# Performance work log

Measured on AMD Instinct MI355X. Metric: run time of the kernel, lower is better.

The kernel has to match this reference:

```python
import jax, jax.numpy as jnp
import numpy as np

N = 65536      # total nodes
B = 128        # graphs in batch
NP = 512       # nodes per graph (N = B*NP)
E = 524288     # edges, avg degree 8, kept within-graph
DIN = 128      # input feature dim
C = 256        # hidden channels
H = 4          # attention heads
DH = C // H
EPS_NRM = 1e-12  # F.normalize eps (SAGEConv normalize=True)
EPS = 1e-5       # GraphNorm / LayerNorm eps


def _xavier(k, shape):
    lim = np.sqrt(6.0 / (shape[-1] + shape[-2]))
    return jax.random.uniform(k, shape, jnp.float32, -lim, lim)


def setup_inputs() -> dict:
    key = jax.random.key(0)
    ks = jax.random.split(key, 20)
    g = jnp.arange(E) // (E // B)  # graph id per edge
    src = (jax.random.randint(ks[0], (E,), 0, NP) + g * NP).astype(jnp.int32)
    dst = (jax.random.randint(ks[1], (E,), 0, NP) + g * NP).astype(jnp.int32)
    edge_index = jnp.stack([src, dst])
    batch = (jnp.arange(N) // NP).astype(jnp.int32)
    x = jax.random.normal(ks[2], (N, DIN), jnp.float32)
    return dict(
        x=x, edge_index=edge_index, batch=batch,
        l0_lin_l_w=_xavier(ks[3], (C, DIN)), l0_lin_l_b=jnp.zeros((C,), jnp.float32),
        l0_lin_r_w=_xavier(ks[4], (C, DIN)),
        l0_res_w=_xavier(ks[5], (C, DIN)),
        lin_l_w=jnp.stack([_xavier(ks[6 + i], (C, C)) for i in range(3)]),
        lin_l_b=jnp.zeros((3, C), jnp.float32),
        lin_r_w=jnp.stack([_xavier(ks[9 + i], (C, C)) for i in range(3)]),
        gn_w=jnp.ones((4, C), jnp.float32), gn_b=jnp.zeros((4, C), jnp.float32),
        gn_alpha=jnp.ones((4, C), jnp.float32),
        attn_in_w=_xavier(ks[12], (3 * C, C)), attn_in_b=jnp.zeros((3 * C,), jnp.float32),
        attn_out_w=_xavier(ks[13], (C, C)), attn_out_b=jnp.zeros((C,), jnp.float32),
        ln_w=jnp.ones((C,), jnp.float32), ln_b=jnp.zeros((C,), jnp.float32),
        pool_w=_xavier(ks[14], (C, 3 * C)), pool_b=jnp.zeros((C,), jnp.float32),
    )


def _forward(x, src, dst, batch, p):
    (l0_lin_l_w, l0_lin_l_b, l0_lin_r_w, l0_res_w, lin_l_w, lin_l_b, lin_r_w,
     gn_w, gn_b, gn_alpha, attn_in_w, attn_in_b, attn_out_w, attn_out_b,
     ln_w, ln_b, pool_w, pool_b) = p
    gelu = lambda v: jax.nn.gelu(v, approximate=False)  # torch nn.GELU default (erf)
    deg = jnp.maximum(jax.ops.segment_sum(jnp.ones((E,), x.dtype), dst, num_segments=N), 1.0)[:, None]

    def sage(h, w_l, b_l, w_r):
        # SAGEConv(mean aggr, normalize=True): lin_l(mean_j x_j) + lin_r(x_i), then L2-normalize
        agg = jax.ops.segment_sum(h[src], dst, num_segments=N) / deg
        out = agg @ w_l.T + b_l + h @ w_r.T
        return out / jnp.maximum(jnp.linalg.norm(out, axis=-1, keepdims=True), EPS_NRM)

    def graph_norm(h, w, b, alpha):
        # GraphNorm: w * (h - alpha*mean_g) / sqrt(var_g + eps) + b, per-graph per-channel
        mean = (jax.ops.segment_sum(h, batch, num_segments=B) / NP)[batch]
        out = h - alpha * mean
        var = (jax.ops.segment_sum(out * out, batch, num_segments=B) / NP)[batch]
        return w * out / jnp.sqrt(var + EPS) + b

    # GNN blocks (eval mode: dropout = identity); layer 0 has residual projection DIN->C
    h = gelu(graph_norm(sage(x, l0_lin_l_w, l0_lin_l_b, l0_lin_r_w), gn_w[0], gn_b[0], gn_alpha[0]))
    x1 = h + x @ l0_res_w.T
    for i in range(3):
        h = gelu(graph_norm(sage(x1, lin_l_w[i], lin_l_b[i], lin_r_w[i]), gn_w[i + 1], gn_b[i + 1], gn_alpha[i + 1]))
        x1 = h + x1

    # BatchedAttentionBlock: equal-size graphs -> to_dense_batch is a reshape, mask all-true
    xd = x1.reshape(B, NP, C)
    qkv = xd @ attn_in_w.T + attn_in_b
    q, k, v = jnp.split(qkv, 3, axis=-1)
    to_h = lambda t: t.reshape(B, NP, H, DH).transpose(0, 2, 1, 3)
    q, k, v = to_h(q), to_h(k), to_h(v)
    scores = jnp.einsum('bhqd,bhkd->bhqk', q, k) / np.float32(np.sqrt(DH))
    attn = jax.nn.softmax(scores, axis=-1)
    o = jnp.einsum('bhqk,bhkd->bhqd', attn, v).transpose(0, 2, 1, 3).reshape(B, NP, C)
    o = o @ attn_out_w.T + attn_out_b
    x2 = o.reshape(N, C) + x1

    # LayerNorm(mode='graph'): normalize over all nodes*features of each graph
    xg = x2.reshape(B, NP * C)
    mu = xg.mean(axis=1, keepdims=True)
    cen = xg - mu
    var = (cen * cen).mean(axis=1, keepdims=True)
    x3 = gelu((cen / jnp.sqrt(var + EPS)).reshape(N, C) * ln_w + ln_b)

    # multi-pool (mean/max/sum) + projection -> graph embedding [B, C]
    xp = x3.reshape(B, NP, C)
    pooled = jnp.concatenate([xp.mean(1), xp.max(1), xp.sum(1)], axis=1)
    return pooled @ pool_w.T + pool_b


def reference(x, edge_index, batch, l0_lin_l_w, l0_lin_l_b, l0_lin_r_w, l0_res_w,
              lin_l_w, lin_l_b, lin_r_w, gn_w, gn_b, gn_alpha,
              attn_in_w, attn_in_b, attn_out_w, attn_out_b, ln_w, ln_b, pool_w, pool_b):
    src, dst = edge_index[0], edge_index[1]
    p = (l0_lin_l_w, l0_lin_l_b, l0_lin_r_w, l0_res_w, lin_l_w, lin_l_b, lin_r_w,
         gn_w, gn_b, gn_alpha, attn_in_w, attn_in_b, attn_out_w, attn_out_b,
         ln_w, ln_b, pool_w, pool_b)
    return _forward(x, src, dst, batch, p)
```

## Files before the change

kernel.cpp:

```cpp
#include <hip/hip_runtime.h>


#define N_TOT   65536
#define B_GR    128
#define NP_     512
#define E_TOT   524288
#define EPG     4096
#define DIN_    128
#define C_      256
#define C3_     768
#define H_      4

typedef unsigned int uint;
typedef unsigned short ushort;

#define O_L0LW  0u
#define O_L0LB  32768u
#define O_L0RW  33024u
#define O_L0RES 65792u
#define O_LWL   98560u
#define O_LBL   295168u
#define O_LWR   295936u
#define O_GNW   492544u
#define O_GNB   493568u
#define O_GNA   494592u
#define O_AIW   495616u
#define O_AIB   692224u
#define O_AOW   692992u
#define O_AOB   758528u
#define O_LNW   758784u
#define O_LNB   759040u
#define O_PLW   759296u
#define O_PLB   955904u
#define TOTALP  956160u

typedef __attribute__((ext_vector_type(8))) short bf16x8_t;
typedef __attribute__((ext_vector_type(4))) float f32x4_t;

__device__ __forceinline__ float bf2f(ushort u){ union{uint i; float f;} v; v.i = ((uint)u) << 16; return v.f; }
__device__ __forceinline__ ushort f2bf(float f){
  union{float f; uint u;} v; v.f = f;
  uint u = v.u;
  u += 0x7fffu + ((u >> 16) & 1u);
  return (ushort)(u >> 16);
}
__device__ __forceinline__ uint pack2(float a, float b){ return (uint)f2bf(a) | ((uint)f2bf(b) << 16); }
__device__ __forceinline__ float u2f_lo(uint u){ union{uint i; float f;} v; v.i = u << 16; return v.f; }
__device__ __forceinline__ float u2f_hi(uint u){ union{uint i; float f;} v; v.i = u & 0xffff0000u; return v.f; }
__device__ __forceinline__ float gelu_f(float x){ return 0.5f * x * (1.0f + erff(x * 0.70710678118654752440f)); }
__device__ __forceinline__ float wredsum(float v){
  #pragma unroll
  for (int off = 32; off; off >>= 1) v += __shfl_xor(v, off, 64);
  return v;
}

__global__ void probe_dtype(const uint* __restrict__ gnw_raw, uint* __restrict__ flag){
  if (threadIdx.x == 0 && blockIdx.x == 0)
    *flag = (gnw_raw[0] == 0x3F800000u) ? 1u : 0u;
}

struct Seg { const void* p; uint ofs; };
struct CvtArgs { Seg s[19]; };

__global__ __launch_bounds__(256) void cvt_params(CvtArgs a, ushort* __restrict__ pb,
                                                  const uint* __restrict__ flag){
  uint gi = blockIdx.x * 256u + threadIdx.x;
  if (gi >= TOTALP) return;
  int lo = 0;
  #pragma unroll
  for (int s = 1; s < 18; ++s) if (gi >= a.s[s].ofs) lo = s;
  uint rel = gi - a.s[lo].ofs;
  pb[gi] = (*flag) ? f2bf(((const float*)a.s[lo].p)[rel]) : ((const ushort*)a.s[lo].p)[rel];
}

__global__ __launch_bounds__(256) void cvt_flat(const void* __restrict__ in, ushort* __restrict__ out,
                                                const uint* __restrict__ flag){
  uint i = blockIdx.x * 256u + threadIdx.x;
  out[i] = (*flag) ? f2bf(((const float*)in)[i]) : ((const ushort*)in)[i];
}

__global__ void deg_count(const int* __restrict__ dst, uint* __restrict__ deg){
  int e = blockIdx.x * 256 + threadIdx.x;
  atomicAdd(&deg[dst[e]], 1u);
}

__global__ __launch_bounds__(512) void scan_deg(const uint* __restrict__ deg,
    uint* __restrict__ rowptr, uint* __restrict__ cursor)
{
  __shared__ uint s[512];
  const int g = blockIdx.x, tid = threadIdx.x;
  uint v = deg[g * NP_ + tid];
  s[tid] = v;
  __syncthreads();
  #pragma unroll
  for (int off = 1; off < 512; off <<= 1) {
    uint t = (tid >= off) ? s[tid - off] : 0u;
    __syncthreads();
    s[tid] += t;
    __syncthreads();
  }
  uint p = g * EPG + (s[tid] - v);
  rowptr[g * NP_ + tid] = p;
  cursor[g * NP_ + tid] = p;
}

__global__ void scatter_edges(const int* __restrict__ src, const int* __restrict__ dst,
    uint* __restrict__ cursor, int* __restrict__ csr)
{
  int e = blockIdx.x * 256 + threadIdx.x;
  uint p = atomicAdd(&cursor[dst[e]], 1u);
  csr[p] = src[e];
}

template<int D>
__global__ __launch_bounds__(256) void sage_agg_csr(const ushort* __restrict__ X,
    const int* __restrict__ csr, const uint* __restrict__ rowptr,
    const uint* __restrict__ deg, ushort* __restrict__ agg)
{
  constexpr int CPL = D / 64;
  const int tid = threadIdx.x, lane = tid & 63, wave = tid >> 6;
  const int n = blockIdx.x * 4 + wave;
  const uint start = rowptr[n];
  const uint dg = deg[n];
  const int co = lane * CPL;
  float acc[CPL];
  #pragma unroll
  for (int k = 0; k < CPL; ++k) acc[k] = 0.0f;

  auto addrow = [&](int s) {
    const ushort* r = X + (size_t)s * D + co;
    if constexpr (CPL == 2) {
      uint u = *(const uint*)r;
      acc[0] += u2f_lo(u); acc[1] += u2f_hi(u);
    } else {
      uint2 u = *(const uint2*)r;
      acc[0] += u2f_lo(u.x); acc[1] += u2f_hi(u.x);
      acc[2] += u2f_lo(u.y); acc[3] += u2f_hi(u.y);
    }
  };

  uint j = 0;
  for (; j + 4 <= dg; j += 4) {
    int s0 = csr[start + j],     s1 = csr[start + j + 1];
    int s2 = csr[start + j + 2], s3 = csr[start + j + 3];
    addrow(s0); addrow(s1); addrow(s2); addrow(s3);
  }
  for (; j < dg; ++j) addrow(csr[start + j]);

  float inv = 1.0f / (float)(dg < 1u ? 1u : dg);
  ushort* op = agg + (size_t)n * D + co;
  if constexpr (CPL == 2) {
    *(uint*)op = pack2(acc[0] * inv, acc[1] * inv);
  } else {
    uint2 o; o.x = pack2(acc[0] * inv, acc[1] * inv);
    o.y = pack2(acc[2] * inv, acc[3] * inv);
    *(uint2*)op = o;
  }
}

#define CS_P 260
template<bool DUAL, bool RN, bool LN>
__global__ __launch_bounds__(256, 4) void gemm_mfma(
    const ushort* __restrict__ A1, int lda1, const ushort* __restrict__ W1,
    const ushort* __restrict__ A2, int lda2, const ushort* __restrict__ W2,
    const ushort* __restrict__ bias, const ushort* addend,
    ushort* out, int K, int ldOut,
    float* __restrict__ m1, float* __restrict__ m2, float* __restrict__ st2)
{
  __shared__ __align__(16) unsigned char smem[34816];
  ushort* As = (ushort*)smem;
  float*  Cs = (float*)smem;
  const int tid = threadIdx.x;
  const int lane = tid & 63, wave = tid >> 6;
  const int lr = lane & 15, quad = lane >> 4;
  const int m0 = blockIdx.x * 64;
  const int n0b = blockIdx.y * 256;
  const int n0 = n0b + wave * 64;
  const int KP = K + 8;
  f32x4_t acc[4][4];
  #pragma unroll
  for (int rt = 0; rt < 4; ++rt)
    #pragma unroll
    for (int ct = 0; ct < 4; ++ct) acc[rt][ct] = (f32x4_t){0.f, 0.f, 0.f, 0.f};

  const int lpr = K >> 3;
  const int rpp = 256 / lpr;
  const int passes = 64 / rpp;
  const int tr = tid / lpr, tc = (tid % lpr) * 8;

  for (int p = 0; p < passes; ++p) {
    int row = p * rpp + tr;
    *(bf16x8_t*)(As + row * KP + tc) =
        *(const bf16x8_t*)(A1 + (size_t)(m0 + row) * lda1 + tc);
  }
  __syncthreads();
  {
    const ushort* wp = W1 + (size_t)(n0 + lr) * K + quad * 8;
    for (int kb = 0; kb < K; kb += 32) {
      bf16x8_t a[4], b[4];
      #pragma unroll
      for (int ct = 0; ct < 4; ++ct) b[ct] = *(const bf16x8_t*)(wp + (size_t)(ct * 16) * K + kb);
      #pragma unroll
      for (int rt = 0; rt < 4; ++rt)
        a[rt] = *(const bf16x8_t*)(As + (rt * 16 + lr) * KP + kb + quad * 8);
      #pragma unroll
      for (int rt = 0; rt < 4; ++rt)
        #pragma unroll
        for (int ct = 0; ct < 4; ++ct)
          acc[rt][ct] = __builtin_amdgcn_mfma_f32_16x16x32_bf16(a[rt], b[ct], acc[rt][ct], 0, 0, 0);
    }
  }
  __syncthreads();
  if constexpr (DUAL) {
    for (int p = 0; p < passes; ++p) {
      int row = p * rpp + tr;
      *(bf16x8_t*)(As + row * KP + tc) =
          *(const bf16x8_t*)(A2 + (size_t)(m0 + row) * lda2 + tc);
    }
    __syncthreads();
    const ushort* wp = W2 + (size_t)(n0 + lr) * K + quad * 8;
    for (int kb = 0; kb < K; kb += 32) {
      bf16x8_t a[4], b[4];
      #pragma unroll
      for (int ct = 0; ct < 4; ++ct) b[ct] = *(const bf16x8_t*)(wp + (size_t)(ct * 16) * K + kb);
      #pragma unroll
      for (int rt = 0; rt < 4; ++rt)
        a[rt] = *(const bf16x8_t*)(As + (rt * 16 + lr) * KP + kb + quad * 8);
      #pragma unroll
      for (int rt = 0; rt < 4; ++rt)
        #pragma unroll
        for (int ct = 0; ct < 4; ++ct)
          acc[rt][ct] = __builtin_amdgcn_mfma_f32_16x16x32_bf16(a[rt], b[ct], acc[rt][ct], 0, 0, 0);
    }
    __syncthreads();
  }

  float bvs[4];
  if (RN && bias) {
    #pragma unroll
    for (int ct = 0; ct < 4; ++ct) bvs[ct] = bf2f(bias[n0 + ct * 16 + lr]);
  }
  float bvL[4] = {0.f, 0.f, 0.f, 0.f};
  if (!RN && bias) {
    #pragma unroll
    for (int j = 0; j < 4; ++j) bvL[j] = bf2f(bias[n0b + lane * 4 + j]);
  }
  float a1s[4] = {0.f, 0.f, 0.f, 0.f}, a2s[4] = {0.f, 0.f, 0.f, 0.f};
  float sln = 0.0f, qln = 0.0f;
  #pragma unroll
  for (int round = 0; round < 2; ++round) {
    #pragma unroll
    for (int rt2 = 0; rt2 < 2; ++rt2) {
      int rt = round * 2 + rt2;
      #pragma unroll
      for (int ct = 0; ct < 4; ++ct)
        #pragma unroll
        for (int r = 0; r < 4; ++r) {
          float v = acc[rt][ct][r];
          if constexpr (RN) v += bias ? bvs[ct] : 0.0f;
          Cs[(rt2 * 16 + quad * 4 + r) * CS_P + wave * 64 + ct * 16 + lr] = v;
        }
    }
    __syncthreads();
    #pragma unroll
    for (int it = 0; it < 8; ++it) {
      int row = wave * 8 + it;
      float4 v = *(const float4*)(Cs + row * CS_P + lane * 4);
      int grow = m0 + round * 32 + row;
      size_t ob = (size_t)grow * ldOut + n0b + lane * 4;
      if constexpr (RN) {
        float ss = v.x*v.x + v.y*v.y + v.z*v.z + v.w*v.w;
        ss = wredsum(ss);
        float inv = 1.0f / fmaxf(sqrtf(ss), 1e-12f);
        float r0 = v.x * inv, r1 = v.y * inv, r2 = v.z * inv, r3 = v.w * inv;
        a1s[0] += r0; a1s[1] += r1; a1s[2] += r2; a1s[3] += r3;
        a2s[0] += r0*r0; a2s[1] += r1*r1; a2s[2] += r2*r2; a2s[3] += r3*r3;
        uint2 o; o.x = pack2(r0, r1); o.y = pack2(r2, r3);
        *(uint2*)(out + ob) = o;
      } else {
        float r0 = v.x + bvL[0], r1 = v.y + bvL[1], r2 = v.z + bvL[2], r3 = v.w + bvL[3];
        if (addend) {
          uint2 ad = *(const uint2*)(addend + ob);
          r0 += u2f_lo(ad.x); r1 += u2f_hi(ad.x);
          r2 += u2f_lo(ad.y); r3 += u2f_hi(ad.y);
        }
        if constexpr (LN) {
          sln += r0 + r1 + r2 + r3;
          qln += r0*r0 + r1*r1 + r2*r2 + r3*r3;
        }
        uint2 o; o.x = pack2(r0, r1); o.y = pack2(r2, r3);
        *(uint2*)(out + ob) = o;
      }
    }
    __syncthreads();
  }
  if constexpr (RN) {
    const int g = m0 >> 9;
    #pragma unroll
    for (int k = 0; k < 4; ++k) {
      atomicAdd(&m1[g*C_ + lane * 4 + k], a1s[k]);
      atomicAdd(&m2[g*C_ + lane * 4 + k], a2s[k]);
    }
  }
  if constexpr (LN) {
    const int g = m0 >> 9;
    sln = wredsum(sln); qln = wredsum(qln);
    if (lane == 0) {
      atomicAdd(&st2[g * 2], sln);
      atomicAdd(&st2[g * 2 + 1], qln);
    }
  }
}

__global__ __launch_bounds__(256) void gn_gelu_add(const ushort* __restrict__ h,
    const ushort* res,
    const float* __restrict__ m1, const float* __restrict__ m2,
    const ushort* __restrict__ gw, const ushort* __restrict__ gb, const ushort* __restrict__ ga,
    ushort* out)
{
  size_t b4 = ((size_t)blockIdx.x * 256 + threadIdx.x) * 4;
  int c = (int)(b4 & (C_ - 1));
  int n = (int)(b4 >> 8);
  int g = n >> 9;
  uint2 hv = *(const uint2*)(h + b4);
  uint2 rv = *(const uint2*)(res + b4);
  float hh[4] = {u2f_lo(hv.x), u2f_hi(hv.x), u2f_lo(hv.y), u2f_hi(hv.y)};
  float rr[4] = {u2f_lo(rv.x), u2f_hi(rv.x), u2f_lo(rv.y), u2f_hi(rv.y)};
  float oo[4];
  #pragma unroll
  for (int j = 0; j < 4; ++j) {
    int cc = c + j;
    float a  = bf2f(ga[cc]);
    float mm = m1[g*C_ + cc] * (1.0f / 512.0f);
    float q2 = m2[g*C_ + cc] * (1.0f / 512.0f);
    float var = q2 - a * (2.0f - a) * mm * mm;
    float xo = hh[j] - a * mm;
    float y = bf2f(gw[cc]) * xo * rsqrtf(var + 1e-5f) + bf2f(gb[cc]);
    oo[j] = gelu_f(y) + rr[j];
  }
  uint2 ov; ov.x = pack2(oo[0], oo[1]); ov.y = pack2(oo[2], oo[3]);
  *(uint2*)(out + b4) = ov;
}

#define KS_P 72
#define VT_P 520
#define PW_P 40
__device__ __forceinline__ int vswz(int c){ return ((c >> 3) & 7) << 3; }
__global__ __launch_bounds__(512, 2) void attn_kernel(ushort* __restrict__ qkv)
{
  __shared__ ushort Ks[NP_ * KS_P];
  __shared__ ushort Vt[64 * VT_P];
  __shared__ ushort Pw[8][16 * PW_P];
  const int bid = blockIdx.x;
  const int g = bid >> 2, h = bid & 3;
  const int tid = threadIdx.x, lane = tid & 63, wave = tid >> 6;
  const int lr = lane & 15, quad = lane >> 4;
  const size_t base = (size_t)g * NP_ * C3_;
  const int qoff = h * 64, koff = C_ + h * 64, voff = 2 * C_ + h * 64;
  for (int idx = tid; idx < NP_ * 64; idx += 512) {
    int j = idx >> 6, c = idx & 63;
    const ushort* row = qkv + base + (size_t)j * C3_;
    Ks[j * KS_P + c] = row[koff + c];
    Vt[c * VT_P + (j ^ vswz(c))] = row[voff + c];
  }
  __syncthreads();
  ushort* pw = &Pw[wave][0];
  const int q0 = wave * 64;
  for (int qt = 0; qt < 4; ++qt) {
    const int qr = q0 + qt * 16;
    const ushort* qp = qkv + base + (size_t)(qr + lr) * C3_ + qoff + quad * 8;
    bf16x8_t qa0 = *(const bf16x8_t*)(qp);
    bf16x8_t qa1 = *(const bf16x8_t*)(qp + 32);
    f32x4_t s[32];
    #pragma unroll
    for (int t = 0; t < 32; ++t) {
      const ushort* kp = Ks + (size_t)(t * 16 + lr) * KS_P + quad * 8;
      bf16x8_t b0 = *(const bf16x8_t*)(kp);
      bf16x8_t b1 = *(const bf16x8_t*)(kp + 32);
      f32x4_t a = (f32x4_t){0.f, 0.f, 0.f, 0.f};
      a = __builtin_amdgcn_mfma_f32_16x16x32_bf16(qa0, b0, a, 0, 0, 0);
      a = __builtin_amdgcn_mfma_f32_16x16x32_bf16(qa1, b1, a, 0, 0, 0);
      s[t] = a;
    }
    float invv[4];
    #pragma unroll
    for (int r = 0; r < 4; ++r) {
      float m = s[0][r];
      #pragma unroll
      for (int t = 1; t < 32; ++t) m = fmaxf(m, s[t][r]);
      #pragma unroll
      for (int off = 8; off; off >>= 1) m = fmaxf(m, __shfl_xor(m, off, 64));
      float sm = 0.0f;
      #pragma unroll
      for (int t = 0; t < 32; ++t) {
        float e = __expf((s[t][r] - m) * 0.125f);
        s[t][r] = e; sm += e;
      }
      #pragma unroll
      for (int off = 8; off; off >>= 1) sm += __shfl_xor(sm, off, 64);
      invv[r] = 1.0f / sm;
    }
    f32x4_t o[4];
    #pragma unroll
    for (int t = 0; t < 4; ++t) o[t] = (f32x4_t){0.f, 0.f, 0.f, 0.f};
    for (int kc = 0; kc < 16; ++kc) {
      #pragma unroll
      for (int half = 0; half < 2; ++half) {
        int t = kc * 2 + half;
        #pragma unroll
        for (int r = 0; r < 4; ++r)
          pw[(quad * 4 + r) * PW_P + half * 16 + lr] = f2bf(s[t][r] * invv[r]);
      }
      __threadfence_block();
      bf16x8_t pa = *(const bf16x8_t*)(pw + lr * PW_P + quad * 8);
      #pragma unroll
      for (int nt = 0; nt < 4; ++nt) {
        int vrow = nt * 16 + lr;
        const ushort* vp = Vt + (size_t)vrow * VT_P + ((kc * 32 + quad * 8) ^ vswz(vrow));
        bf16x8_t b = *(const bf16x8_t*)(vp);
        o[nt] = __builtin_amdgcn_mfma_f32_16x16x32_bf16(pa, b, o[nt], 0, 0, 0);
      }
    }
    #pragma unroll
    for (int nt = 0; nt < 4; ++nt)
      #pragma unroll
      for (int r = 0; r < 4; ++r)
        qkv[base + (size_t)(qr + quad * 4 + r) * C3_ + koff + nt * 16 + lr] =
            f2bf(o[nt][r]);
  }
}

__global__ __launch_bounds__(256) void ln_gelu(const ushort* __restrict__ x2, const float* __restrict__ st2,
    const ushort* __restrict__ lw, const ushort* __restrict__ lb, ushort* __restrict__ x3)
{
  __shared__ float musd[2];
  size_t b4 = ((size_t)blockIdx.x * 256 + threadIdx.x) * 4;
  int c = (int)(b4 & (C_ - 1));
  int g = (int)(b4 >> 17);
  if (threadIdx.x == 0) {
    float S = st2[g * 2], Q = st2[g * 2 + 1];
    float mu = S * (1.0f / (NP_ * C_));
    float var = Q * (1.0f / (NP_ * C_)) - mu * mu;
    musd[0] = mu; musd[1] = rsqrtf(var + 1e-5f);
  }
  __syncthreads();
  float mu = musd[0], rs = musd[1];
  uint2 v = *(const uint2*)(x2 + b4);
  float vv[4] = {u2f_lo(v.x), u2f_hi(v.x), u2f_lo(v.y), u2f_hi(v.y)};
  float oo[4];
  #pragma unroll
  for (int j = 0; j < 4; ++j) {
    int cc = c + j;
    float y = (vv[j] - mu) * rs * bf2f(lw[cc]) + bf2f(lb[cc]);
    oo[j] = gelu_f(y);
  }
  uint2 ov; ov.x = pack2(oo[0], oo[1]); ov.y = pack2(oo[2], oo[3]);
  *(uint2*)(x3 + b4) = ov;
}

__global__ __launch_bounds__(256) void pool_part(const ushort* __restrict__ x3,
    float* __restrict__ psum, float* __restrict__ pmax)
{
  const int g = blockIdx.x, sl = blockIdx.y, c = threadIdx.x;
  const ushort* p = x3 + ((size_t)g * NP_ + sl * 64) * C_ + c;
  float s = 0.0f, mx = -3.0e38f;
  #pragma unroll 4
  for (int r = 0; r < 64; ++r) {
    float v = bf2f(p[(size_t)r * C_]);
    s += v; mx = fmaxf(mx, v);
  }
  psum[((size_t)g * 8 + sl) * C_ + c] = s;
  pmax[((size_t)g * 8 + sl) * C_ + c] = mx;
}

__global__ __launch_bounds__(256) void final_gemm(const float* __restrict__ psum,
    const float* __restrict__ pmax,
    const ushort* __restrict__ W, const ushort* __restrict__ b, void* __restrict__ out,
    const uint* __restrict__ flag)
{
  __shared__ float pl[C3_];
  const int g = blockIdx.x, c = threadIdx.x;
  float s = 0.0f, mx = -3.0e38f;
  #pragma unroll
  for (int sl = 0; sl < 8; ++sl) {
    s += psum[((size_t)g * 8 + sl) * C_ + c];
    mx = fmaxf(mx, pmax[((size_t)g * 8 + sl) * C_ + c]);
  }
  pl[c] = s * (1.0f / 512.0f);
  pl[C_ + c] = mx;
  pl[2 * C_ + c] = s;
  __syncthreads();
  float acc = bf2f(b[c]);
  const ushort* wr = W + (size_t)c * C3_;
  for (int k = 0; k < C3_; k += 2) {
    uint wv = *(const uint*)(wr + k);
    acc += pl[k] * u2f_lo(wv) + pl[k + 1] * u2f_hi(wv);
  }
  if (*flag) ((float*)out)[g * C_ + c] = acc;
  else       ((ushort*)out)[g * C_ + c] = f2bf(acc);
}

extern "C" void kernel_launch(void* const* d_in, const int* in_sizes, int n_in,
                              void* d_out, int out_size, void* d_ws, size_t ws_size,
                              hipStream_t stream)
{
  const int* ei   = (const int*)d_in[1];
  const int* srcp = ei;
  const int* dstp = ei + E_TOT;

  const size_t NC = (size_t)N_TOT * C_;
  const size_t NEEDED = (4ull << 20) + 4 * NC * sizeof(ushort);
  if (ws_size < NEEDED) return;

  unsigned char* wsb = (unsigned char*)d_ws;
  uint*   deg    = (uint*)wsb;
  float*  mbuf   = (float*)(wsb + (256u << 10));
  float*  st2    = (float*)(wsb + (1280u << 10));
  uint*   flag   = (uint*)(wsb + (1288u << 10));
  ushort* PB     = (ushort*)(wsb + (1792u << 10));
  ushort* S0     = (ushort*)(wsb + (4u << 20));
  ushort* S1     = S0 + NC;
  ushort* S2     = S1 + NC;
  ushort* S3     = S2 + NC;
  ushort* qkvb   = S1;
  ushort* XB     = S3;
  unsigned char* s3hi = (unsigned char*)(S3 + (size_t)N_TOT * DIN_);
  int*  csr    = (int*)s3hi;
  uint* rowptr = (uint*)(s3hi + (2u << 20));
  uint* cursor = (uint*)(s3hi + (2u << 20) + (256u << 10));
  float* psum  = (float*)S2;
  float* pmax  = psum + (size_t)B_GR * 8 * C_;

  probe_dtype<<<1, 1, 0, stream>>>((const uint*)d_in[10], flag);
  CvtArgs ca;
  ca.s[0]  = { d_in[3],  O_L0LW };  ca.s[1]  = { d_in[4],  O_L0LB };
  ca.s[2]  = { d_in[5],  O_L0RW };  ca.s[3]  = { d_in[6],  O_L0RES };
  ca.s[4]  = { d_in[7],  O_LWL  };  ca.s[5]  = { d_in[8],  O_LBL  };
  ca.s[6]  = { d_in[9],  O_LWR  };  ca.s[7]  = { d_in[10], O_GNW  };
  ca.s[8]  = { d_in[11], O_GNB  };  ca.s[9]  = { d_in[12], O_GNA  };
  ca.s[10] = { d_in[13], O_AIW  };  ca.s[11] = { d_in[14], O_AIB  };
  ca.s[12] = { d_in[15], O_AOW  };  ca.s[13] = { d_in[16], O_AOB  };
  ca.s[14] = { d_in[17], O_LNW  };  ca.s[15] = { d_in[18], O_LNB  };
  ca.s[16] = { d_in[19], O_PLW  };  ca.s[17] = { d_in[20], O_PLB  };
  ca.s[18] = { nullptr,  TOTALP };
  cvt_params<<<(TOTALP + 255) / 256, 256, 0, stream>>>(ca, PB, flag);
  cvt_flat<<<(N_TOT * DIN_) / 256, 256, 0, stream>>>(d_in[0], XB, flag);

  hipMemsetAsync(deg, 0, N_TOT * sizeof(uint), stream);
  hipMemsetAsync(mbuf, 0, (1u << 20) + 1024, stream);

  deg_count<<<E_TOT / 256, 256, 0, stream>>>(dstp, deg);
  scan_deg<<<B_GR, 512, 0, stream>>>(deg, rowptr, cursor);
  scatter_edges<<<E_TOT / 256, 256, 0, stream>>>(srcp, dstp, cursor, csr);

  const size_t MSZ = (size_t)B_GR * C_;
  {
    float* m1 = mbuf;
    float* m2 = mbuf + MSZ * 4;
    sage_agg_csr<DIN_><<<N_TOT / 4, 256, 0, stream>>>(XB, csr, rowptr, deg, S1);
    gemm_mfma<true, true, false><<<dim3(N_TOT / 64, 1), 256, 0, stream>>>(
        S1, DIN_, PB + O_L0LW, XB, DIN_, PB + O_L0RW, PB + O_L0LB, nullptr, S2, DIN_, C_, m1, m2, nullptr);
    gemm_mfma<false, false, false><<<dim3(N_TOT / 64, 1), 256, 0, stream>>>(
        XB, DIN_, PB + O_L0RES, nullptr, 0, nullptr, nullptr, nullptr, S0, DIN_, C_, nullptr, nullptr, nullptr);
    gn_gelu_add<<<(N_TOT * C_) / 1024, 256, 0, stream>>>(S2, S0, m1, m2,
        PB + O_GNW, PB + O_GNB, PB + O_GNA, S0);
  }

  for (int i = 0; i < 3; ++i) {
    float* m1 = mbuf + MSZ * (i + 1);
    float* m2 = mbuf + MSZ * 4 + MSZ * (i + 1);
    sage_agg_csr<C_><<<N_TOT / 4, 256, 0, stream>>>(S0, csr, rowptr, deg, S1);
    gemm_mfma<true, true, false><<<dim3(N_TOT / 64, 1), 256, 0, stream>>>(
        S1, C_, PB + O_LWL + (size_t)i * C_ * C_, S0, C_, PB + O_LWR + (size_t)i * C_ * C_,
        PB + O_LBL + i * C_, nullptr, S2, C_, C_, m1, m2, nullptr);
    gn_gelu_add<<<(N_TOT * C_) / 1024, 256, 0, stream>>>(S2, S0, m1, m2,
        PB + O_GNW + (i + 1) * C_, PB + O_GNB + (i + 1) * C_, PB + O_GNA + (i + 1) * C_, S0);
  }

  gemm_mfma<false, false, false><<<dim3(N_TOT / 64, 3), 256, 0, stream>>>(
      S0, C_, PB + O_AIW, nullptr, 0, nullptr, PB + O_AIB, nullptr, qkvb, C_, C3_, nullptr, nullptr, nullptr);
  attn_kernel<<<B_GR * H_, 512, 0, stream>>>(qkvb);
  gemm_mfma<false, false, true><<<dim3(N_TOT / 64, 1), 256, 0, stream>>>(
      qkvb + C_, C3_, PB + O_AOW, nullptr, 0, nullptr, PB + O_AOB, S0, S0, C_, C_, nullptr, nullptr, st2);

  ln_gelu<<<(N_TOT * C_) / 1024, 256, 0, stream>>>(S0, st2, PB + O_LNW, PB + O_LNB, S1);

  pool_part<<<dim3(B_GR, 8), 256, 0, stream>>>(S1, psum, pmax);
  final_gemm<<<B_GR, 256, 0, stream>>>(psum, pmax, PB + O_PLW, PB + O_PLB, d_out, flag);
}
```

Before: 1.024 ms.

## Transpose attention MFMAs to keep softmax probabilities in registers

The QK^T MFMA operands are swapped so each lane holds one query's scores across keys. Softmax reductions then mostly happen within registers, with only two shuffles. The P matrix is packed directly into bf16 MFMA operands instead of round-tripping through a per-wave shared-memory buffer, and V is stored with a key permutation that matches this register layout. Staging loads are vectorised and outputs are written as 8-byte stores. The cost is a more intricate permuted V layout that must match the MFMA output mapping exactly.

New measurement: 1.522 ms. 1.49x slower.

```diff
diff --git a/kernel.cpp b/kernel.cpp
--- a/kernel.cpp
+++ b/kernel.cpp
@@ -344,27 +344,36 @@
 
 #define KS_P 72
 #define VT_P 520
-#define PW_P 40
 __device__ __forceinline__ int vswz(int c){ return ((c >> 3) & 7) << 3; }
+__device__ __forceinline__ int vperm(int j){
+  return (j & 0x1E0) | (((j >> 2) & 3) << 3) | (((j >> 4) & 1) << 2) | (j & 3);
+}
 __global__ __launch_bounds__(512, 2) void attn_kernel(ushort* __restrict__ qkv)
 {
-  __shared__ ushort Ks[NP_ * KS_P];
-  __shared__ ushort Vt[64 * VT_P];
-  __shared__ ushort Pw[8][16 * PW_P];
+  __shared__ __align__(16) ushort Ks[NP_ * KS_P];
+  __shared__ __align__(16) ushort Vt[64 * VT_P];
   const int bid = blockIdx.x;
   const int g = bid >> 2, h = bid & 3;
   const int tid = threadIdx.x, lane = tid & 63, wave = tid >> 6;
   const int lr = lane & 15, quad = lane >> 4;
   const size_t base = (size_t)g * NP_ * C3_;
   const int qoff = h * 64, koff = C_ + h * 64, voff = 2 * C_ + h * 64;
-  for (int idx = tid; idx < NP_ * 64; idx += 512) {
-    int j = idx >> 6, c = idx & 63;
+
+  for (int idx = tid; idx < NP_ * 8; idx += 512) {
+    int j = idx >> 3, c8 = (idx & 7) << 3;
     const ushort* row = qkv + base + (size_t)j * C3_;
-    Ks[j * KS_P + c] = row[koff + c];
-    Vt[c * VT_P + (j ^ vswz(c))] = row[voff + c];
+    bf16x8_t kv = *(const bf16x8_t*)(row + koff + c8);
+    *(bf16x8_t*)(Ks + j * KS_P + c8) = kv;
+    bf16x8_t vv = *(const bf16x8_t*)(row + voff + c8);
+    int sj = vperm(j);
+    #pragma unroll
+    for (int m = 0; m < 8; ++m) {
+      int c = c8 + m;
+      Vt[c * VT_P + (sj ^ vswz(c))] = ((const ushort*)&vv)[m];
+    }
   }
   __syncthreads();
-  ushort* pw = &Pw[wave][0];
+
   const int q0 = wave * 64;
   for (int qt = 0; qt < 4; ++qt) {
     const int qr = q0 + qt * 16;
@@ -378,55 +387,60 @@
       bf16x8_t b0 = *(const bf16x8_t*)(kp);
       bf16x8_t b1 = *(const bf16x8_t*)(kp + 32);
       f32x4_t a = (f32x4_t){0.f, 0.f, 0.f, 0.f};
-      a = __builtin_amdgcn_mfma_f32_16x16x32_bf16(qa0, b0, a, 0, 0, 0);
-      a = __builtin_amdgcn_mfma_f32_16x16x32_bf16(qa1, b1, a, 0, 0, 0);
+      a = __builtin_amdgcn_mfma_f32_16x16x32_bf16(b0, qa0, a, 0, 0, 0);
+      a = __builtin_amdgcn_mfma_f32_16x16x32_bf16(b1, qa1, a, 0, 0, 0);
       s[t] = a;
     }
-    float invv[4];
-    #pragma unroll
-    for (int r = 0; r < 4; ++r) {
-      float m = s[0][r];
-      #pragma unroll
-      for (int t = 1; t < 32; ++t) m = fmaxf(m, s[t][r]);
-      #pragma unroll
-      for (int off = 8; off; off >>= 1) m = fmaxf(m, __shfl_xor(m, off, 64));
-      float sm = 0.0f;
-      #pragma unroll
-      for (int t = 0; t < 32; ++t) {
-        float e = __expf((s[t][r] - m) * 0.125f);
-        s[t][r] = e; sm += e;
+    float m0 = s[0][0], m1 = s[0][1], m2 = s[0][2], m3 = s[0][3];
+    #pragma unroll
+    for (int t = 1; t < 32; ++t) {
+      m0 = fmaxf(m0, s[t][0]); m1 = fmaxf(m1, s[t][1]);
+      m2 = fmaxf(m2, s[t][2]); m3 = fmaxf(m3, s[t][3]);
+    }
+    float m = fmaxf(fmaxf(m0, m1), fmaxf(m2, m3));
+    m = fmaxf(m, __shfl_xor(m, 16, 64));
+    m = fmaxf(m, __shfl_xor(m, 32, 64));
+    float sm0 = 0.f, sm1 = 0.f, sm2 = 0.f, sm3 = 0.f;
+    #pragma unroll
+    for (int t = 0; t < 32; ++t) {
+      float e0 = __expf((s[t][0] - m) * 0.125f);
+      float e1 = __expf((s[t][1] - m) * 0.125f);
+      float e2 = __expf((s[t][2] - m) * 0.125f);
+      float e3 = __expf((s[t][3] - m) * 0.125f);
+      s[t][0] = e0; s[t][1] = e1; s[t][2] = e2; s[t][3] = e3;
+      sm0 += e0; sm1 += e1; sm2 += e2; sm3 += e3;
+    }
+    float sm = (sm0 + sm1) + (sm2 + sm3);
+    sm += __shfl_xor(sm, 16, 64);
+    sm += __shfl_xor(sm, 32, 64);
+    float inv = 1.0f / sm;
+
+    f32x4_t o[4];
+    #pragma unroll
+    for (int dt = 0; dt < 4; ++dt) o[dt] = (f32x4_t){0.f, 0.f, 0.f, 0.f};
+    #pragma unroll
+    for (int u = 0; u < 16; ++u) {
+      union { uint w[4]; bf16x8_t v; } pb;
+      pb.w[0] = pack2(s[2*u][0] * inv,     s[2*u][1] * inv);
+      pb.w[1] = pack2(s[2*u][2] * inv,     s[2*u][3] * inv);
+      pb.w[2] = pack2(s[2*u+1][0] * inv,   s[2*u+1][1] * inv);
+      pb.w[3] = pack2(s[2*u+1][2] * inv,   s[2*u+1][3] * inv);
+      #pragma unroll
+      for (int dt = 0; dt < 4; ++dt) {
+        int vrow = dt * 16 + lr;
+        const ushort* vp = Vt + (size_t)vrow * VT_P + ((u * 32 + quad * 8) ^ vswz(vrow));
+        bf16x8_t av = *(const bf16x8_t*)vp;
+        o[dt] = __builtin_amdgcn_mfma_f32_16x16x32_bf16(av, pb.v, o[dt], 0, 0, 0);
       }
-      #pragma unroll
-      for (int off = 8; off; off >>= 1) sm += __shfl_xor(sm, off, 64);
-      invv[r] = 1.0f / sm;
-    }
-    f32x4_t o[4];
-    #pragma unroll
-    for (int t = 0; t < 4; ++t) o[t] = (f32x4_t){0.f, 0.f, 0.f, 0.f};
-    for (int kc = 0; kc < 16; ++kc) {
-      #pragma unroll
-      for (int half = 0; half < 2; ++half) {
-        int t = kc * 2 + half;
-        #pragma unroll
-        for (int r = 0; r < 4; ++r)
-          pw[(quad * 4 + r) * PW_P + half * 16 + lr] = f2bf(s[t][r] * invv[r]);
-      }
-      __threadfence_block();
-      bf16x8_t pa = *(const bf16x8_t*)(pw + lr * PW_P + quad * 8);
-      #pragma unroll
-      for (int nt = 0; nt < 4; ++nt) {
-        int vrow = nt * 16 + lr;
-        const ushort* vp = Vt + (size_t)vrow * VT_P + ((kc * 32 + quad * 8) ^ vswz(vrow));
-        bf16x8_t b = *(const bf16x8_t*)(vp);
-        o[nt] = __builtin_amdgcn_mfma_f32_16x16x32_bf16(pa, b, o[nt], 0, 0, 0);
-      }
-    }
-    #pragma unroll
-    for (int nt = 0; nt < 4; ++nt)
-      #pragma unroll
-      for (int r = 0; r < 4; ++r)
-        qkv[base + (size_t)(qr + quad * 4 + r) * C3_ + koff + nt * 16 + lr] =
-            f2bf(o[nt][r]);
+    }
+    ushort* orow = qkv + base + (size_t)(qr + lr) * C3_ + koff + quad * 4;
+    #pragma unroll
+    for (int dt = 0; dt < 4; ++dt) {
+      uint2 ov;
+      ov.x = pack2(o[dt][0], o[dt][1]);
+      ov.y = pack2(o[dt][2], o[dt][3]);
+      *(uint2*)(orow + dt * 16) = ov;
+    }
   }
 }
 
```
